# Performance work log

Measured on AMD Instinct MI355X. Metric: run time of the kernel, lower is better.

## Reference

```python
import jax, jax.numpy as jnp
import numpy as np

T = 100000
M = 32
PI_CONST = 3.1415926  # matches the constant used in the original source


def setup_inputs() -> dict:
    key = jax.random.key(0)
    k1, k2, k3, k4, k5, k6 = jax.random.split(key, 6)
    obs_2_T = jax.random.normal(k1, (T,), dtype=jnp.float32)
    obs_1_T_1 = jax.random.normal(k2, (T,), dtype=jnp.float32)
    mean = jax.random.normal(k3, (M,), dtype=jnp.float32)
    # variances must be positive
    var = jax.random.uniform(k4, (M,), dtype=jnp.float32) + jnp.float32(0.5)
    bate = jnp.float32(0.85)
    # pi: valid initial distribution; aij: row-stochastic transition matrix
    pi = jax.nn.softmax(jax.random.normal(k5, (M,), dtype=jnp.float32))
    aij = jax.nn.softmax(jax.random.normal(k6, (M, M), dtype=jnp.float32), axis=-1)
    return {"obs_2_T": obs_2_T, "obs_1_T_1": obs_1_T_1, "mean": mean,
            "var": var, "bate": bate, "pi": pi, "aij": aij}


def reference(obs_2_T, obs_1_T_1, mean, var, bate, pi, aij):
    # Eta[i, j, t] = exp(-(obs2[t] - (mean[j] + bate*(obs1[t] - mean[i]))) / (2*var[j]))
    #               / sqrt(2*pi*var[j])
    # (NOTE: faithful to the source, which does NOT square the residual.)
    inv2v = 1.0 / (2.0 * var)                      # (m,)
    norm = 1.0 / jnp.sqrt(2.0 * PI_CONST * var)    # (m,)
    # diff: (m_i, m_j, T)
    diff = obs_2_T[None, None, :] - (mean[None, :, None]
                                     + bate * (obs_1_T_1[None, None, :] - mean[:, None, None]))
    Eta = jnp.exp(-diff * inv2v[None, :, None]) * norm[None, :, None]  # (m, m, T)
    Eta_t = jnp.moveaxis(Eta, -1, 0)  # (T, m, m)

    # Normalized forward recursion:
    # t=0: num[i,j] = Eta[i,j,0] * pi[i] * aij[i,j]
    # t>0: num[i,j] = Eta[i,j,t] * Epsilon[t-1,i] * aij[i,j]
    # Gamma[t] = num / sum(num);  Epsilon[t,j] = sum_i Gamma[t,i,j]
    def step(eps_prev, eta):  # eps_prev: (m,), eta: (m, m)
        num = eta * eps_prev[:, None] * aij
        g = num / jnp.sum(num)
        return jnp.sum(g, axis=0), g

    _, Gamma = jax.lax.scan(step, pi, Eta_t)  # Gamma: (T, m, m)

    # loss = sum_t <Gamma[t], Eta[:, :, t]>
    loss = jnp.sum(Gamma * Eta_t)
    return loss
```

## Files before the change

kernel.cpp:

```cpp
#include <hip/hip_runtime.h>

constexpr int TN   = 100000;
constexpr int NCH  = 2000;
constexpr int CLEN = 50;
constexpr int WARM = 64;
constexpr int WPB  = 4;
constexpr int NBLK = NCH / WPB;
constexpr int MAXS = WARM + CLEN;

constexpr float LOG2E = 1.4426950408889634f;
constexpr float PI_F  = 3.1415926f;

#define ROR(src, N) __int_as_float(__builtin_amdgcn_mov_dpp( \
    __float_as_int(src), 0x120 + (N), 0xF, 0xF, false))

#define ROTS(SRC, R)                                                          \
  float R##1 = ROR(SRC, 1),  R##2 = ROR(SRC, 2),  R##3 = ROR(SRC, 3),         \
        R##4 = ROR(SRC, 4),  R##5 = ROR(SRC, 5),  R##6 = ROR(SRC, 6),         \
        R##7 = ROR(SRC, 7),  R##8 = ROR(SRC, 8),  R##9 = ROR(SRC, 9),         \
        R##10 = ROR(SRC,10), R##11 = ROR(SRC,11), R##12 = ROR(SRC,12),        \
        R##13 = ROR(SRC,13), R##14 = ROR(SRC,14), R##15 = ROR(SRC,15);

#define DOT16(Wr, SRC, R, d0,d1,d2,d3,d4,d5,d6,d7)                            \
  d0 += Wr[0]*(SRC);  d1 += Wr[1]*R##1;   d2 += Wr[2]*R##2;   d3 += Wr[3]*R##3;   \
  d4 += Wr[4]*R##4;   d5 += Wr[5]*R##5;   d6 += Wr[6]*R##6;   d7 += Wr[7]*R##7;   \
  d0 += Wr[8]*R##8;   d1 += Wr[9]*R##9;   d2 += Wr[10]*R##10; d3 += Wr[11]*R##11; \
  d4 += Wr[12]*R##12; d5 += Wr[13]*R##13; d6 += Wr[14]*R##14; d7 += Wr[15]*R##15;

__global__ __launch_bounds__(256, 2) void k_main(
    const float* __restrict__ obs2, const float* __restrict__ obs1,
    const float* __restrict__ mean_p, const float* __restrict__ var_p,
    const float* __restrict__ bate_p, const float* __restrict__ pi_p,
    const float* __restrict__ aij, float* __restrict__ lossbuf)
{
  const int w = threadIdx.x >> 6, lane = threadIdx.x & 63;
  const int wv = blockIdx.x * WPB + w;
  const int i   = lane & 15;
  const int blk = (lane >> 4) & 1;
  const int j   = blk * 16 + i;
  const int ob  = blk * 16;
  const int nb  = 16 - ob;

  __shared__ __align__(16) float Wsh[2][32][32];
  __shared__ float cts[WPB][MAXS + 2];

  {
    const int tid = threadIdx.x;
    const int jj = tid & 31, ig = tid >> 5;
    float vjq  = var_p[jj];
    float i2vq = 0.5f / vjq;
    float norm = rsqrtf(2.0f * PI_F * vjq);
    float Aj   = norm * expf(mean_p[jj] * i2vq);
    float bate = bate_p[0];
#pragma unroll
    for (int m = 0; m < 4; ++m) {
      int ii = ig * 4 + m;
      float Bij = expf(-bate * mean_p[ii] * i2vq);
      float wq = aij[ii * 32 + jj] * Aj * Bij;
      Wsh[0][ii][jj] = wq;
      Wsh[1][ii][jj] = wq * Aj * Bij;
    }
  }

  float vj  = var_p[j];
  float i2v = 0.5f / vj;
  float s_  = i2v;
#pragma unroll
  for (int o = 1; o < 32; o <<= 1) s_ += __shfl_xor(s_, o);
  const float i2vl = i2v * LOG2E;
  const float i2vc = (i2v - s_ * 0.03125f) * LOG2E;

  const int t0 = wv * CLEN;
  const int tw = (t0 > WARM) ? (t0 - WARM) : 0;
  const int n  = t0 + CLEN - tw;
  const int warmsteps = t0 - tw;
  {
    float bate = bate_p[0];
    for (int l = lane; l < n; l += 64)
      cts[w][l] = obs2[tw + l] - bate * obs1[tw + l];
  }
  __syncthreads();

  int dird;
  { int p = __builtin_amdgcn_mov_dpp(i, 0x121, 0xF, 0xF, false);
    dird = (p - i) & 15; }

  float WA[16], WB[16], VA[16], VB[16];
#pragma unroll
  for (int N = 0; N < 16; ++N) {
    int kk = (i + N * dird) & 15;
    WA[N] = Wsh[0][ob + kk][j];
    WB[N] = Wsh[0][nb + kk][j];
    VA[N] = Wsh[1][ob + kk][j];
    VB[N] = Wsh[1][nb + kk][j];
  }

  float y  = (tw == 0) ? pi_p[j] : 0.03125f;
  float y2 = __shfl_xor(y, 16);

  int s = 0;
  for (; s < warmsteps; ++s) {
    float ct = cts[w][s];
    float u  = exp2f(-ct * i2vc);
    ROTS(y, a) ROTS(y2, b)
    float d0=0,d1=0,d2=0,d3=0,d4=0,d5=0,d6=0,d7=0;
    DOT16(WA, y,  a, d0,d1,d2,d3,d4,d5,d6,d7)
    DOT16(WB, y2, b, d0,d1,d2,d3,d4,d5,d6,d7)
    float dot = ((d0+d1)+(d2+d3)) + ((d4+d5)+(d6+d7));
    y = u * dot;
    if ((s & 3) == 3)
      y *= __builtin_amdgcn_rcpf(__int_as_float(
             __builtin_amdgcn_readfirstlane(__float_as_int(y))));
    y2 = __shfl_xor(y, 16);
  }
  float lossacc = 0.f;
  const int h = lane >> 5;
  for (; s < n; ++s) {
    float ct = cts[w][s];
    float u  = exp2f(-ct * i2vl);
    ROTS(y, a) ROTS(y2, b)
    float d0=0,d1=0,d2=0,d3=0,d4=0,d5=0,d6=0,d7=0;
    float e0=0,e1=0,e2=0,e3=0,e4=0,e5=0,e6=0,e7=0;
    DOT16(WA, y,  a, d0,d1,d2,d3,d4,d5,d6,d7)
    DOT16(WB, y2, b, d0,d1,d2,d3,d4,d5,d6,d7)
    DOT16(VA, y,  a, e0,e1,e2,e3,e4,e5,e6,e7)
    DOT16(VB, y2, b, e0,e1,e2,e3,e4,e5,e6,e7)
    float dotW = ((d0+d1)+(d2+d3)) + ((d4+d5)+(d6+d7));
    float dotV = ((e0+e1)+(e2+e3)) + ((e4+e5)+(e6+e7));
    float numj = u * dotW;
    float n2j  = (u * u) * dotV;
    float red  = h ? n2j : numj;
#pragma unroll
    for (int o = 1; o < 32; o <<= 1) red += __shfl_xor(red, o);
    float cross = __shfl_xor(red, 32);
    float S  = h ? cross : red;
    float N2 = h ? red   : cross;
    float rs = __builtin_amdgcn_rcpf(S);
    lossacc += N2 * rs;
    y  = numj * rs;
    y2 = __shfl_xor(y, 16);
  }
  if (lane == 0) lossbuf[wv] = lossacc;
}

__global__ __launch_bounds__(256) void k_finish(const float* __restrict__ lb,
                                                float* __restrict__ out)
{
  const int tid = threadIdx.x;
  float v = 0.f;
  for (int l = tid; l < NCH; l += 256) v += lb[l];
#pragma unroll
  for (int o = 1; o < 64; o <<= 1) v += __shfl_xor(v, o);
  __shared__ float part[4];
  if ((tid & 63) == 0) part[tid >> 6] = v;
  __syncthreads();
  if (tid == 0) out[0] = part[0] + part[1] + part[2] + part[3];
}

extern "C" void kernel_launch(void* const* d_in, const int* in_sizes, int n_in,
                              void* d_out, int out_size, void* d_ws, size_t ws_size,
                              hipStream_t stream)
{
  (void)in_sizes; (void)n_in; (void)ws_size; (void)out_size;
  const float* obs2 = (const float*)d_in[0];
  const float* obs1 = (const float*)d_in[1];
  const float* mean = (const float*)d_in[2];
  const float* var  = (const float*)d_in[3];
  const float* bate = (const float*)d_in[4];
  const float* pi   = (const float*)d_in[5];
  const float* aij  = (const float*)d_in[6];
  float* lb  = (float*)d_ws;
  float* out = (float*)d_out;

  k_main  <<<NBLK, 256, 0, stream>>>(obs2, obs1, mean, var, bate, pi, aij, lb);
  k_finish<<<1,    256, 0, stream>>>(lb, out);
}
```

Measured before the change: 109.9 us.

## Split k-reduction across wave halves, shorten chunks and warmup, raise occupancy

```diff
diff --git a/kernel.cpp b/kernel.cpp
--- a/kernel.cpp
+++ b/kernel.cpp
@@ -1,9 +1,9 @@
 #include <hip/hip_runtime.h>
 
 constexpr int TN   = 100000;
-constexpr int NCH  = 2000;
-constexpr int CLEN = 50;
-constexpr int WARM = 64;
+constexpr int NCH  = 2500;
+constexpr int CLEN = 40;
+constexpr int WARM = 32;
 constexpr int WPB  = 4;
 constexpr int NBLK = NCH / WPB;
 constexpr int MAXS = WARM + CLEN;
@@ -21,13 +21,21 @@
         R##10 = ROR(SRC,10), R##11 = ROR(SRC,11), R##12 = ROR(SRC,12),        \
         R##13 = ROR(SRC,13), R##14 = ROR(SRC,14), R##15 = ROR(SRC,15);
 
-#define DOT16(Wr, SRC, R, d0,d1,d2,d3,d4,d5,d6,d7)                            \
-  d0 += Wr[0]*(SRC);  d1 += Wr[1]*R##1;   d2 += Wr[2]*R##2;   d3 += Wr[3]*R##3;   \
-  d4 += Wr[4]*R##4;   d5 += Wr[5]*R##5;   d6 += Wr[6]*R##6;   d7 += Wr[7]*R##7;   \
-  d0 += Wr[8]*R##8;   d1 += Wr[9]*R##9;   d2 += Wr[10]*R##10; d3 += Wr[11]*R##11; \
-  d4 += Wr[12]*R##12; d5 += Wr[13]*R##13; d6 += Wr[14]*R##14; d7 += Wr[15]*R##15;
+#define DOT16(Wr, SRC, R, dd)                                                 \
+  float dd;                                                                   \
+  { float q0 = Wr[0]*(SRC)  + Wr[4]*R##4;                                     \
+    float q1 = Wr[1]*R##1   + Wr[5]*R##5;                                     \
+    float q2 = Wr[2]*R##2   + Wr[6]*R##6;                                     \
+    float q3 = Wr[3]*R##3   + Wr[7]*R##7;                                     \
+    q0 += Wr[8]*R##8;   q1 += Wr[9]*R##9;                                     \
+    q2 += Wr[10]*R##10; q3 += Wr[11]*R##11;                                   \
+    q0 += Wr[12]*R##12; q1 += Wr[13]*R##13;                                   \
+    q2 += Wr[14]*R##14; q3 += Wr[15]*R##15;                                   \
+    dd = (q0 + q1) + (q2 + q3); }
 
-__global__ __launch_bounds__(256, 2) void k_main(
+#define RING16(v) { v += ROR(v,1); v += ROR(v,2); v += ROR(v,4); v += ROR(v,8); }
+
+__global__ __launch_bounds__(256, 3) void k_main(
     const float* __restrict__ obs2, const float* __restrict__ obs1,
     const float* __restrict__ mean_p, const float* __restrict__ var_p,
     const float* __restrict__ bate_p, const float* __restrict__ pi_p,
@@ -35,11 +43,10 @@
 {
   const int w = threadIdx.x >> 6, lane = threadIdx.x & 63;
   const int wv = blockIdx.x * WPB + w;
-  const int i   = lane & 15;
-  const int blk = (lane >> 4) & 1;
-  const int j   = blk * 16 + i;
-  const int ob  = blk * 16;
-  const int nb  = 16 - ob;
+  const int i  = lane & 15;
+  const int h  = lane >> 5;
+  const int j  = lane & 31;
+  const int kb = h * 16;
 
   __shared__ __align__(16) float Wsh[2][32][32];
   __shared__ float cts[WPB][MAXS + 2];
@@ -85,60 +92,56 @@
   { int p = __builtin_amdgcn_mov_dpp(i, 0x121, 0xF, 0xF, false);
     dird = (p - i) & 15; }
 
-  float WA[16], WB[16], VA[16], VB[16];
+  float Wr[16], Vr[16];
 #pragma unroll
   for (int N = 0; N < 16; ++N) {
     int kk = (i + N * dird) & 15;
-    WA[N] = Wsh[0][ob + kk][j];
-    WB[N] = Wsh[0][nb + kk][j];
-    VA[N] = Wsh[1][ob + kk][j];
-    VB[N] = Wsh[1][nb + kk][j];
+    Wr[N] = Wsh[0][kb + kk][j];
+    Vr[N] = Wsh[1][kb + kk][j];
   }
 
-  float y  = (tw == 0) ? pi_p[j] : 0.03125f;
-  float y2 = __shfl_xor(y, 16);
+  const bool takeT = (((lane >> 4) & 1) ^ h) != 0;
+
+  float y = (tw == 0) ? pi_p[j] : 0.03125f;
+  float t = __shfl_xor(y, 16);
+  float ysrc = takeT ? t : y;
 
   int s = 0;
   for (; s < warmsteps; ++s) {
     float ct = cts[w][s];
     float u  = exp2f(-ct * i2vc);
-    ROTS(y, a) ROTS(y2, b)
-    float d0=0,d1=0,d2=0,d3=0,d4=0,d5=0,d6=0,d7=0;
-    DOT16(WA, y,  a, d0,d1,d2,d3,d4,d5,d6,d7)
-    DOT16(WB, y2, b, d0,d1,d2,d3,d4,d5,d6,d7)
-    float dot = ((d0+d1)+(d2+d3)) + ((d4+d5)+(d6+d7));
+    ROTS(ysrc, a)
+    DOT16(Wr, ysrc, a, pW)
+    float dot = pW + __shfl_xor(pW, 32);
     y = u * dot;
     if ((s & 3) == 3)
       y *= __builtin_amdgcn_rcpf(__int_as_float(
              __builtin_amdgcn_readfirstlane(__float_as_int(y))));
-    y2 = __shfl_xor(y, 16);
+    t = __shfl_xor(y, 16);
+    ysrc = takeT ? t : y;
   }
   float lossacc = 0.f;
-  const int h = lane >> 5;
   for (; s < n; ++s) {
     float ct = cts[w][s];
     float u  = exp2f(-ct * i2vl);
-    ROTS(y, a) ROTS(y2, b)
-    float d0=0,d1=0,d2=0,d3=0,d4=0,d5=0,d6=0,d7=0;
-    float e0=0,e1=0,e2=0,e3=0,e4=0,e5=0,e6=0,e7=0;
-    DOT16(WA, y,  a, d0,d1,d2,d3,d4,d5,d6,d7)
-    DOT16(WB, y2, b, d0,d1,d2,d3,d4,d5,d6,d7)
-    DOT16(VA, y,  a, e0,e1,e2,e3,e4,e5,e6,e7)
-    DOT16(VB, y2, b, e0,e1,e2,e3,e4,e5,e6,e7)
-    float dotW = ((d0+d1)+(d2+d3)) + ((d4+d5)+(d6+d7));
-    float dotV = ((e0+e1)+(e2+e3)) + ((e4+e5)+(e6+e7));
+    ROTS(ysrc, a)
+    DOT16(Wr, ysrc, a, pW)
+    DOT16(Vr, ysrc, a, pV)
+    float dotW = pW + __shfl_xor(pW, 32);
+    float dotV = pV + __shfl_xor(pV, 32);
     float numj = u * dotW;
     float n2j  = (u * u) * dotV;
     float red  = h ? n2j : numj;
-#pragma unroll
-    for (int o = 1; o < 32; o <<= 1) red += __shfl_xor(red, o);
+    RING16(red)
+    red += __shfl_xor(red, 16);
     float cross = __shfl_xor(red, 32);
     float S  = h ? cross : red;
     float N2 = h ? red   : cross;
     float rs = __builtin_amdgcn_rcpf(S);
     lossacc += N2 * rs;
-    y  = numj * rs;
-    y2 = __shfl_xor(y, 16);
+    y = numj * rs;
+    t = __shfl_xor(y, 16);
+    ysrc = takeT ? t : y;
   }
   if (lane == 0) lossbuf[wv] = lossacc;
 }
```

After: 94.34 us. -14.1%, faster.
